# Kernel optimization log

Hardware: AMD Instinct MI355X
Metric: run time of the kernel (lower is better)

The kernel has to match this reference:

```python
import jax, jax.numpy as jnp
import numpy as np

B, DIM = 8, 2048          # batch, dim == N == C (forced by module's shape constraints)
NUM_HEADS = 8


def setup_inputs() -> dict:
    key = jax.random.key(0)
    k1, k2 = jax.random.split(key)
    x = jax.random.normal(k1, (B, DIM, DIM), dtype=jnp.float32)      # (B, N, C), N==C==dim
    Wq = jax.random.normal(k2, (DIM, DIM), dtype=jnp.float32) * 0.02  # Conv1d(dim,dim,1) weight, no bias
    return {"x": x, "Wq": Wq, "H": 64, "W": 32}


def reference(x, Wq, H, W):
    Bb, N, C = x.shape
    scale = (C // NUM_HEADS) ** -0.5  # qk_scale=None -> head_dim**-0.5
    # self.q: Conv1d(dim, dim, kernel_size=1) applied to x (B, N, C) -> channel axis is N
    q = jnp.einsum('oi,bil->bol', Wq, x)             # (B, N, C)
    # sr_ratio == 1: k_ = x (no spatial reduction; self.sr not constructed)
    attn = jnp.einsum('bnc,bmc->bnm', q, x) * scale  # (B, N, N)
    # self.rwmp = MaxPool1d(dim) with row length N==dim -> max over last axis, keepdim
    m = jnp.max(attn, axis=-1, keepdims=True)        # (B, N, 1)
    # self.v = AvgPool1d(dim) on x^T (B, C, N), N==dim -> mean over tokens
    v = jnp.mean(x, axis=1, keepdims=True)           # (B, 1, C)
    y = m * v                                        # (B, N, 1) @ (B, 1, C) outer product
    # .transpose(1, 2).reshape(B, N, C)  (valid since N == C)
    return jnp.swapaxes(y, 1, 2).reshape(Bb, N, C)
```

## Files before the change

kernel.cpp:

```cpp
#include <hip/hip_runtime.h>

#define DIM 2048
#define NB 8

typedef _Float16 f16;
typedef __attribute__((ext_vector_type(8))) _Float16 f16x8;
typedef __attribute__((ext_vector_type(4))) _Float16 f16x4;
typedef __attribute__((ext_vector_type(2))) _Float16 f16x2;
typedef __attribute__((ext_vector_type(4))) float f32x4;
typedef __attribute__((ext_vector_type(4))) unsigned u32x4;

__device__ __forceinline__ unsigned fkey(float f) {
    unsigned u = __float_as_uint(f);
    return (u & 0x80000000u) ? ~u : (u | 0x80000000u);
}
__device__ __forceinline__ float fdecode(unsigned k) {
    return (k & 0x80000000u) ? __uint_as_float(k ^ 0x80000000u)
                             : __uint_as_float(~k);
}

__device__ __forceinline__ void gld_lds16(const f16* g, f16* l) {
    __builtin_amdgcn_global_load_lds(
        (const __attribute__((address_space(1))) unsigned*)g,
        (__attribute__((address_space(3))) unsigned*)l, 16, 0, 0);
}

__global__ __launch_bounds__(256) void k_convert(const float* __restrict__ src,
                                                 f16* __restrict__ dst, int n4) {
    int i = blockIdx.x * 256 + threadIdx.x;
    if (i >= n4) return;
    f32x4 v = ((const f32x4*)src)[i];
    ((f16x4*)dst)[i] = __builtin_convertvector(v, f16x4);
}

__global__ __launch_bounds__(256) void k_prep(const float* __restrict__ x,
                                              f16* __restrict__ Xf,
                                              float* __restrict__ vsum) {
    const int b  = blockIdx.z;
    const int c0 = blockIdx.x * 1024 + threadIdx.x * 4;
    const int n0 = blockIdx.y * 64;
    const float* px = x  + ((size_t)b * DIM + n0) * DIM + c0;
    f16*         pd = Xf + ((size_t)b * DIM + n0) * DIM + c0;
    f32x4 s = (f32x4){0.f, 0.f, 0.f, 0.f};
    #pragma unroll 8
    for (int n = 0; n < 64; ++n) {
        f32x4 v = *(const f32x4*)(px + (size_t)n * DIM);
        *(f16x4*)(pd + (size_t)n * DIM) = __builtin_convertvector(v, f16x4);
        s += v;
    }
    atomicAdd(&vsum[b * DIM + c0 + 0], s.x);
    atomicAdd(&vsum[b * DIM + c0 + 1], s.y);
    atomicAdd(&vsum[b * DIM + c0 + 2], s.z);
    atomicAdd(&vsum[b * DIM + c0 + 3], s.w);
}

__global__ __launch_bounds__(256) void k_colsum(const float* __restrict__ x,
                                                float* __restrict__ vsum) {
    int b = blockIdx.z;
    int c = blockIdx.x * 256 + threadIdx.x;
    int n0 = blockIdx.y * (DIM / 8);
    const float* p = x + ((size_t)b * DIM + n0) * DIM + c;
    float s = 0.f;
    #pragma unroll 8
    for (int n = 0; n < DIM / 8; ++n) s += p[(size_t)n * DIM];
    atomicAdd(&vsum[b * DIM + c], s);
}

__device__ __forceinline__ void gemm128_core(const f16* __restrict__ A,
                                             const f16* __restrict__ Bt,
                                             int br, int bc,
                                             f16* As, f16* Bs,
                                             f32x4 acc[4][4]) {
    const int tid  = threadIdx.x;
    const int ln   = tid & 63;
    const int wv   = tid >> 6;
    const int l15  = ln & 15;
    const int quad = ln >> 4;
    const int wr   = (wv >> 1) * 64;
    const int wc   = (wv & 1) * 64;
    const int lrow = ln >> 3;
    const int lg   = (ln & 7) ^ lrow;
    const int swz  = l15 & 7;

    const f16* gA = A  + (size_t)(br * 128 + wv * 32 + lrow) * DIM + lg * 8;
    const f16* gB = Bt + (size_t)(bc * 128 + wv * 32 + lrow) * DIM + lg * 8;
    f16* lA = As + wv * 2048 + ln * 8;
    f16* lB = Bs + wv * 2048 + ln * 8;

    #pragma unroll
    for (int i = 0; i < 4; ++i)
        #pragma unroll
        for (int j = 0; j < 4; ++j)
            acc[i][j] = (f32x4){0.f, 0.f, 0.f, 0.f};

    for (int kt = 0; kt < DIM / 64; ++kt) {
        __syncthreads();
        #pragma unroll
        for (int u = 0; u < 4; ++u) {
            gld_lds16(gA + (size_t)u * 8 * DIM, lA + u * 512);
            gld_lds16(gB + (size_t)u * 8 * DIM, lB + u * 512);
        }
        gA += 64; gB += 64;
        __syncthreads();
        #pragma unroll
        for (int kk = 0; kk < 2; ++kk) {
            const int s = (kk * 4 + quad) ^ swz;
            f16x8 af[4], bf[4];
            #pragma unroll
            for (int i = 0; i < 4; ++i)
                af[i] = *(const f16x8*)(As + (wr + i * 16 + l15) * 64 + s * 8);
            #pragma unroll
            for (int j = 0; j < 4; ++j)
                bf[j] = *(const f16x8*)(Bs + (wc + j * 16 + l15) * 64 + s * 8);
            #pragma unroll
            for (int i = 0; i < 4; ++i)
                #pragma unroll
                for (int j = 0; j < 4; ++j)
                    acc[i][j] = __builtin_amdgcn_mfma_f32_16x16x32_f16(af[i], bf[j], acc[i][j], 0, 0, 0);
        }
    }
}

__global__ __launch_bounds__(256) void k_gram(const f16* __restrict__ Xall,
                                              f16* __restrict__ Gall,
                                              unsigned long xStride,
                                              unsigned long gStride) {
    const int b = blockIdx.y;
    const f16* X = Xall + (size_t)b * xStride;
    f16* G = Gall + (size_t)b * gStride;

    int t = blockIdx.x;
    int br = (int)((sqrtf(8.f * t + 1.f) - 1.f) * 0.5f);
    while ((br + 1) * (br + 2) / 2 <= t) ++br;
    while (br * (br + 1) / 2 > t) --br;
    int bc = t - br * (br + 1) / 2;

    __shared__ __align__(16) f16 smem[128 * 136];
    f16* As = smem;
    f16* Bs = smem + 8192;
    f32x4 acc[4][4];
    gemm128_core(X, X, br, bc, As, Bs, acc);

    const int tid = threadIdx.x;
    const int ln = tid & 63;
    const int wv = tid >> 6;
    const int wr = (wv >> 1) * 64, wc = (wv & 1) * 64;
    const int l15 = ln & 15, quad = ln >> 4;

    #pragma unroll
    for (int i = 0; i < 4; ++i)
        #pragma unroll
        for (int j = 0; j < 4; ++j)
            #pragma unroll
            for (int r = 0; r < 4; ++r) {
                int row = br * 128 + wr + i * 16 + quad * 4 + r;
                int col = bc * 128 + wc + j * 16 + l15;
                G[(size_t)row * DIM + col] = (f16)acc[i][j][r];
            }

    if (br != bc) {
        __syncthreads();
        f16* T = smem;
        #pragma unroll
        for (int i = 0; i < 4; ++i)
            #pragma unroll
            for (int j = 0; j < 4; ++j)
                #pragma unroll
                for (int h = 0; h < 2; ++h) {
                    int row = wr + i * 16 + quad * 4 + h * 2;
                    int col = wc + j * 16 + l15;
                    f16x2 v = {(f16)acc[i][j][h * 2], (f16)acc[i][j][h * 2 + 1]};
                    *(f16x2*)(T + col * 136 + row) = v;
                }
        __syncthreads();
        #pragma unroll
        for (int p = 0; p < 8; ++p) {
            int ch = p * 256 + tid;
            int rt = ch >> 4, seg = ch & 15;
            f16x8 v = *(const f16x8*)(T + rt * 136 + seg * 8);
            *(f16x8*)(G + (size_t)(bc * 128 + rt) * DIM + br * 128 + seg * 8) = v;
        }
    }
}

__global__ __launch_bounds__(256) void k_attn(const f16* __restrict__ Wq,
                                              const f16* __restrict__ Gall,
                                              unsigned* __restrict__ mkey,
                                              unsigned long gStride, int batchBase) {
    const int bz = blockIdx.z;
    const int bi = bz + batchBase;
    const f16* G = Gall + (size_t)bz * gStride;
    const int br = blockIdx.y, bc = blockIdx.x;

    __shared__ __align__(16) f16 smem[2 * 128 * 64];
    f16* As = smem;
    f16* Bs = smem + 8192;
    f32x4 acc[4][4];
    gemm128_core(Wq, G, br, bc, As, Bs, acc);

    const int lane = threadIdx.x & 63;
    const int wave = threadIdx.x >> 6;
    const int wr = (wave >> 1) * 64;
    const int l15 = lane & 15, quad = lane >> 4;
    const float scale = 0.0625f;

    #pragma unroll
    for (int i = 0; i < 4; ++i) {
        #pragma unroll
        for (int r = 0; r < 4; ++r) {
            float v = acc[i][0][r];
            v = fmaxf(v, acc[i][1][r]);
            v = fmaxf(v, acc[i][2][r]);
            v = fmaxf(v, acc[i][3][r]);
            #pragma unroll
            for (int m = 1; m <= 8; m <<= 1)
                v = fmaxf(v, __shfl_xor(v, m, 64));
            if (l15 == 0) {
                int row = br * 128 + wr + i * 16 + quad * 4 + r;
                atomicMax(&mkey[(size_t)bi * DIM + row], fkey(scale * v));
            }
        }
    }
}

__global__ __launch_bounds__(256) void k_final(const float* __restrict__ vsum,
                                               const unsigned* __restrict__ mkey,
                                               float* __restrict__ out) {
    int gid = blockIdx.x * 256 + threadIdx.x;
    int b   = gid >> 20;
    int rem = gid & 1048575;
    int i   = rem >> 9;
    int jq  = rem & 511;
    float v = vsum[(b << 11) + i] * (1.f / 2048.f);
    u32x4 k = ((const u32x4*)mkey)[(b << 9) + jq];
    f32x4 o;
    o.x = v * fdecode(k.x);
    o.y = v * fdecode(k.y);
    o.z = v * fdecode(k.z);
    o.w = v * fdecode(k.w);
    ((f32x4*)out)[gid] = o;
}

extern "C" void kernel_launch(void* const* d_in, const int* in_sizes, int n_in,
                              void* d_out, int out_size, void* d_ws, size_t ws_size,
                              hipStream_t stream) {
    const float* x  = (const float*)d_in[0];
    const float* Wq = (const float*)d_in[1];
    float* out = (float*)d_out;
    char* ws = (char*)d_ws;

    const size_t elems = (size_t)DIM * DIM;
    unsigned* mkey = (unsigned*)ws;
    float*    vsum = (float*)(ws + 65536);
    f16*      Wqf  = (f16*)(ws + 131072);
    f16*      Xf   = (f16*)(ws + 131072 + elems * 2);

    const size_t need1 = 131072 + elems * 2 * (1 + NB + NB);
    const size_t need2 = 131072 + elems * 2 * (1 + NB + 1);

    hipMemsetAsync(ws, 0, 131072, stream);
    k_convert<<<4096, 256, 0, stream>>>(Wq, Wqf, (int)(elems / 4));

    if (ws_size >= need1) {
        f16* G = Xf + NB * elems;
        k_prep<<<dim3(2, 32, NB), 256, 0, stream>>>(x, Xf, vsum);
        k_gram<<<dim3(136, NB), 256, 0, stream>>>(Xf, G, elems, elems);
        k_attn<<<dim3(16, 16, NB), 256, 0, stream>>>(Wqf, G, mkey, elems, 0);
    } else if (ws_size >= need2) {
        f16* G = Xf + NB * elems;
        k_prep<<<dim3(2, 32, NB), 256, 0, stream>>>(x, Xf, vsum);
        for (int b = 0; b < NB; ++b) {
            k_gram<<<dim3(136, 1), 256, 0, stream>>>(Xf + (size_t)b * elems, G, 0, 0);
            k_attn<<<dim3(16, 16, 1), 256, 0, stream>>>(Wqf, G, mkey, 0, b);
        }
    } else {
        f16* G = Xf + elems;
        k_colsum<<<dim3(8, 8, 8), 256, 0, stream>>>(x, vsum);
        for (int b = 0; b < NB; ++b) {
            k_convert<<<4096, 256, 0, stream>>>(x + (size_t)b * elems, Xf, (int)(elems / 4));
            k_gram<<<dim3(136, 1), 256, 0, stream>>>(Xf, G, 0, 0);
            k_attn<<<dim3(16, 16, 1), 256, 0, stream>>>(Wqf, G, mkey, 0, b);
        }
    }
    k_final<<<32768, 256, 0, stream>>>(vsum, mkey, out);
}
```

Before: 530.7 us.

## Replace attention GEMM with 256x256-tile, 8-wave pipelined MFMA kernel

```diff
diff --git a/kernel.cpp b/kernel.cpp
--- a/kernel.cpp
+++ b/kernel.cpp
@@ -2,6 +2,7 @@
 
 #define DIM 2048
 #define NB 8
+#define NT (DIM / 64)
 
 typedef _Float16 f16;
 typedef __attribute__((ext_vector_type(8))) _Float16 f16x8;
@@ -24,6 +25,14 @@
         (const __attribute__((address_space(1))) unsigned*)g,
         (__attribute__((address_space(3))) unsigned*)l, 16, 0, 0);
 }
+
+#define BAR() asm volatile("s_barrier" ::: "memory")
+#define WAITLGKM0()                                            \
+    do {                                                       \
+        asm volatile("s_waitcnt lgkmcnt(0)" ::: "memory");     \
+        __builtin_amdgcn_sched_barrier(0);                     \
+    } while (0)
+#define WAITVM(N) asm volatile("s_waitcnt vmcnt(" #N ")" ::: "memory")
 
 __global__ __launch_bounds__(256) void k_convert(const float* __restrict__ src,
                                                  f16* __restrict__ dst, int n4) {
@@ -183,40 +192,131 @@
     }
 }
 
-__global__ __launch_bounds__(256) void k_attn(const f16* __restrict__ Wq,
-                                              const f16* __restrict__ Gall,
-                                              unsigned* __restrict__ mkey,
-                                              unsigned long gStride, int batchBase) {
-    const int bz = blockIdx.z;
-    const int bi = bz + batchBase;
-    const f16* G = Gall + (size_t)bz * gStride;
-    const int br = blockIdx.y, bc = blockIdx.x;
-
-    __shared__ __align__(16) f16 smem[2 * 128 * 64];
-    f16* As = smem;
-    f16* Bs = smem + 8192;
-    f32x4 acc[4][4];
-    gemm128_core(Wq, G, br, bc, As, Bs, acc);
-
-    const int lane = threadIdx.x & 63;
-    const int wave = threadIdx.x >> 6;
-    const int wr = (wave >> 1) * 64;
-    const int l15 = lane & 15, quad = lane >> 4;
+__global__ __launch_bounds__(512, 2)
+void k_attn256(const f16* __restrict__ Wq, const f16* __restrict__ Gall,
+               unsigned* __restrict__ mkey, unsigned long gStride, int batchBase) {
+    __shared__ __align__(16) f16 sm[2][2][256 * 64];
+
+    const int q  = gridDim.x >> 3;
+    const int w  = (blockIdx.x & 7) * q + (blockIdx.x >> 3);
+    const int zi = w >> 6;
+    const int br = (w >> 3) & 7;
+    const int bc = w & 7;
+    const f16* A  = Wq;
+    const f16* Bt = Gall + (size_t)zi * gStride;
+    const int bi = batchBase + zi;
+
+    const int tid  = threadIdx.x;
+    const int ln   = tid & 63;
+    const int wv   = tid >> 6;
+    const int wm   = wv >> 2;
+    const int wn   = wv & 3;
+    const int l15  = ln & 15;
+    const int quad = ln >> 4;
+    const int swz  = l15 & 7;
+    const int cc0  = ((quad) ^ swz) * 8;
+    const int cc1  = ((4 | quad) ^ swz) * 8;
+    const int lrow = ln >> 3;
+    const int lchunk = (ln & 7) ^ lrow;
+
+    f32x4 acc[8][4];
+    #pragma unroll
+    for (int i = 0; i < 8; ++i)
+        #pragma unroll
+        for (int j = 0; j < 4; ++j) acc[i][j] = (f32x4){0.f, 0.f, 0.f, 0.f};
+
+    auto stage = [&](int t, int s) {
+        if (t >= NT) return;
+        const int p = t & 1;
+        const f16* src; int rowb; f16* L;
+        if (s == 0 || s == 3) { src = A;  rowb = br * 256; L = (f16*)sm[p][0]; }
+        else                  { src = Bt; rowb = bc * 256; L = (f16*)sm[p][1]; }
+        const int h  = (s >= 2) ? 1 : 0;
+        const int r0 = h * 128 + wv * 16;
+        const f16* gp = src + (size_t)(rowb + r0 + lrow) * DIM + t * 64 + lchunk * 8;
+        f16* lp = L + r0 * 64 + ln * 8;
+        gld_lds16(gp, lp);
+        gld_lds16(gp + (size_t)8 * DIM, lp + 512);
+    };
+
+    f16x8 af[4][2], bl[2][2], bh[2][2];
+
+    auto loadA = [&](int qm, const f16* LA) {
+        #pragma unroll
+        for (int i = 0; i < 4; ++i) {
+            const f16* pa = LA + (qm * 128 + wm * 64 + i * 16 + l15) * 64;
+            af[i][0] = *(const f16x8*)(pa + cc0);
+            af[i][1] = *(const f16x8*)(pa + cc1);
+        }
+    };
+    auto loadB = [&](int qn, const f16* LB, f16x8 (&bf)[2][2]) {
+        #pragma unroll
+        for (int j = 0; j < 2; ++j) {
+            const f16* pb = LB + (qn * 128 + wn * 32 + j * 16 + l15) * 64;
+            bf[j][0] = *(const f16x8*)(pb + cc0);
+            bf[j][1] = *(const f16x8*)(pb + cc1);
+        }
+    };
+    auto mfmaQ = [&](int qm, int qn, f16x8 (&a)[4][2], f16x8 (&bf)[2][2]) {
+        __builtin_amdgcn_s_setprio(1);
+        #pragma unroll
+        for (int i = 0; i < 4; ++i)
+            #pragma unroll
+            for (int j = 0; j < 2; ++j)
+                #pragma unroll
+                for (int kk = 0; kk < 2; ++kk)
+                    acc[qm * 4 + i][qn * 2 + j] = __builtin_amdgcn_mfma_f32_16x16x32_f16(
+                        a[i][kk], bf[j][kk], acc[qm * 4 + i][qn * 2 + j], 0, 0, 0);
+        __builtin_amdgcn_s_setprio(0);
+        __builtin_amdgcn_sched_barrier(0);
+    };
+
+    stage(0, 0); stage(0, 1); stage(0, 2); stage(0, 3);
+    WAITVM(4);
+    stage(1, 0); stage(1, 1); stage(1, 2);
+    WAITVM(6);
+    BAR();
+
+    for (int t = 0; t < NT; ++t) {
+        const int p = t & 1;
+        const f16* LA = (const f16*)sm[p][0];
+        const f16* LB = (const f16*)sm[p][1];
+        loadA(0, LA); loadB(0, LB, bl);
+        stage(t + 1, 3);
+        BAR(); WAITLGKM0();
+        mfmaQ(0, 0, af, bl);
+        BAR();
+        loadB(1, LB, bh);
+        stage(t + 2, 0);
+        BAR(); WAITLGKM0();
+        mfmaQ(0, 1, af, bh);
+        BAR();
+        loadA(1, LA);
+        stage(t + 2, 1);
+        BAR(); WAITLGKM0();
+        mfmaQ(1, 1, af, bh);
+        BAR();
+        stage(t + 2, 2);
+        BAR();
+        mfmaQ(1, 0, af, bl);
+        if (t < NT - 2) { WAITVM(6); }
+        else            { WAITVM(0); }
+        BAR();
+    }
+
     const float scale = 0.0625f;
-
     #pragma unroll
-    for (int i = 0; i < 4; ++i) {
+    for (int i = 0; i < 8; ++i) {
+        const int qm = i >> 2, il = i & 3;
         #pragma unroll
         for (int r = 0; r < 4; ++r) {
-            float v = acc[i][0][r];
-            v = fmaxf(v, acc[i][1][r]);
-            v = fmaxf(v, acc[i][2][r]);
-            v = fmaxf(v, acc[i][3][r]);
+            float v = fmaxf(fmaxf(acc[i][0][r], acc[i][1][r]),
+                            fmaxf(acc[i][2][r], acc[i][3][r]));
             #pragma unroll
             for (int m = 1; m <= 8; m <<= 1)
                 v = fmaxf(v, __shfl_xor(v, m, 64));
             if (l15 == 0) {
-                int row = br * 128 + wr + i * 16 + quad * 4 + r;
+                const int row = br * 256 + qm * 128 + wm * 64 + il * 16 + quad * 4 + r;
                 atomicMax(&mkey[(size_t)bi * DIM + row], fkey(scale * v));
             }
         }
@@ -265,13 +365,13 @@
         f16* G = Xf + NB * elems;
         k_prep<<<dim3(2, 32, NB), 256, 0, stream>>>(x, Xf, vsum);
         k_gram<<<dim3(136, NB), 256, 0, stream>>>(Xf, G, elems, elems);
-        k_attn<<<dim3(16, 16, NB), 256, 0, stream>>>(Wqf, G, mkey, elems, 0);
+        k_attn256<<<dim3(512), 512, 0, stream>>>(Wqf, G, mkey, elems, 0);
     } else if (ws_size >= need2) {
         f16* G = Xf + NB * elems;
         k_prep<<<dim3(2, 32, NB), 256, 0, stream>>>(x, Xf, vsum);
         for (int b = 0; b < NB; ++b) {
             k_gram<<<dim3(136, 1), 256, 0, stream>>>(Xf + (size_t)b * elems, G, 0, 0);
-            k_attn<<<dim3(16, 16, 1), 256, 0, stream>>>(Wqf, G, mkey, 0, b);
+            k_attn256<<<dim3(64), 512, 0, stream>>>(Wqf, G, mkey, 0, b);
         }
     } else {
         f16* G = Xf + elems;
@@ -279,7 +379,7 @@
         for (int b = 0; b < NB; ++b) {
             k_convert<<<4096, 256, 0, stream>>>(x + (size_t)b * elems, Xf, (int)(elems / 4));
             k_gram<<<dim3(136, 1), 256, 0, stream>>>(Xf, G, 0, 0);
-            k_attn<<<dim3(16, 16, 1), 256, 0, stream>>>(Wqf, G, mkey, 0, b);
+            k_attn256<<<dim3(64), 512, 0, stream>>>(Wqf, G, mkey, 0, b);
         }
     }
     k_final<<<32768, 256, 0, stream>>>(vsum, mkey, out);
```

After: 499.2 us. 1.06x faster.
